# Kernel tuning notes

Hardware: AMD Instinct MI355X
Metric: run time of the kernel (lower is better)

Reference implementation:

```python
import jax, jax.numpy as jnp
import numpy as np

V, D, H, L, FF, BS = 50257, 1024, 16, 8, 4096, 1024
B, T = 2, 1024
HD = D // H
SCALE = 1.0 / np.sqrt(HD)
STD = 0.02


def setup_inputs() -> dict:
    key = jax.random.key(0)
    ks = jax.random.split(key, 8)
    rn = lambda k, s: (jax.random.normal(k, s, jnp.float32) * STD)
    return {
        'idx': jax.random.randint(ks[0], (B, T), 0, V),
        'tok_emb': rn(ks[1], (V, D)),
        'pos_emb': rn(ks[2], (1, BS, D)),
        'ln1_w': jnp.ones((L, D)), 'ln1_b': jnp.zeros((L, D)),
        'qkv_w': rn(ks[3], (L, 3 * D, D)), 'qkv_b': jnp.zeros((L, 3 * D)),
        'proj_w': rn(ks[4], (L, D, D)), 'proj_b': jnp.zeros((L, D)),
        'ln2_w': jnp.ones((L, D)), 'ln2_b': jnp.zeros((L, D)),
        'fc1_w': rn(ks[5], (L, FF, D)), 'fc1_b': jnp.zeros((L, FF)),
        'fc2_w': rn(ks[6], (L, D, FF)), 'fc2_b': jnp.zeros((L, D)),
        'lnf_w': jnp.ones((D,)), 'lnf_b': jnp.zeros((D,)),
    }


def layernorm(x, w, b, eps=1e-5):
    mu = jnp.mean(x, axis=-1, keepdims=True)
    var = jnp.mean(jnp.square(x - mu), axis=-1, keepdims=True)
    return (x - mu) * jax.lax.rsqrt(var + eps) * w + b


def _forward(idx, tok_emb, pos_emb, ln1_w, ln1_b, qkv_w, qkv_b, proj_w, proj_b,
             ln2_w, ln2_b, fc1_w, fc1_b, fc2_w, fc2_b, lnf_w, lnf_b):
    b, t = idx.shape
    x = tok_emb[idx] + pos_emb[0, :t]           # [B,T,D]; dropout identity in eval
    mask = jnp.tril(jnp.ones((t, t), dtype=bool))  # causal

    def block(x, p):
        l1w, l1b, qw, qb, pw, pb, l2w, l2b, f1w, f1b, f2w, f2b = p
        h = layernorm(x, l1w, l1b)
        qkv = h @ qw.T + qb                      # [B,T,3D]
        qkv = qkv.reshape(b, t, 3, H, HD)
        q, k, v = qkv[:, :, 0], qkv[:, :, 1], qkv[:, :, 2]  # [B,T,H,HD]
        att = jnp.einsum('bqhd,bkhd->bhqk', q, k) * SCALE
        att = jnp.where(mask, att, -jnp.inf)
        att = jax.nn.softmax(att, axis=-1)       # attn dropout identity in eval
        y = jnp.einsum('bhqk,bkhd->bqhd', att, v).reshape(b, t, D)
        x = x + (y @ pw.T + pb)
        h = layernorm(x, l2w, l2b)
        h = jax.nn.gelu(h @ f1w.T + f1b, approximate=False)  # exact GELU as nn.GELU
        x = x + (h @ f2w.T + f2b)
        return x, None

    params = (ln1_w, ln1_b, qkv_w, qkv_b, proj_w, proj_b,
              ln2_w, ln2_b, fc1_w, fc1_b, fc2_w, fc2_b)
    x, _ = jax.lax.scan(block, x, params)
    x = layernorm(x, lnf_w, lnf_b)
    logits = x @ tok_emb.T                       # weight-tied head
    return logits


def reference(idx, tok_emb, pos_emb, ln1_w, ln1_b, qkv_w, qkv_b, proj_w, proj_b,
              ln2_w, ln2_b, fc1_w, fc1_b, fc2_w, fc2_b, lnf_w, lnf_b):
    return _forward(idx, tok_emb, pos_emb, ln1_w, ln1_b, qkv_w, qkv_b, proj_w,
                    proj_b, ln2_w, ln2_b, fc1_w, fc1_b, fc2_w, fc2_b, lnf_w, lnf_b)
```

## Files before the change

### kernel.cpp

```cpp
#include <hip/hip_runtime.h>
#include <cstdint>

#define Dm 1024
#define Tm 1024
#define Bm 2
#define Lm 8
#define FFm 4096
#define Vm 50257
#define Mm (Bm * Tm)
#define VPAD2 50432

typedef __bf16 bf16x8 __attribute__((ext_vector_type(8)));
typedef float f32x4 __attribute__((ext_vector_type(4)));
typedef unsigned short u16;
typedef unsigned int u32;
typedef u16 u16x8 __attribute__((ext_vector_type(8)));
typedef u16 u16x4 __attribute__((ext_vector_type(4)));

__device__ __forceinline__ u16 f2bf(float f) {
  u32 u = __float_as_uint(f);
  u += 0x7FFFu + ((u >> 16) & 1u);
  return (u16)(u >> 16);
}
__device__ __forceinline__ float bf2f(u16 u) {
  return __uint_as_float((u32)u << 16);
}
__device__ __forceinline__ u32 packbf(float lo, float hi) {
  return (u32)f2bf(lo) | ((u32)f2bf(hi) << 16);
}

__device__ __forceinline__ void gload16(const u16* g, u16* l) {
  __builtin_amdgcn_global_load_lds(
      (const __attribute__((address_space(1))) void*)g,
      (__attribute__((address_space(3))) void*)l, 16, 0, 0);
}

__global__ __launch_bounds__(256) void embed_k(
    const int* __restrict__ idx, const float* __restrict__ tok,
    const float* __restrict__ pos, float* __restrict__ x) {
  int m = blockIdx.x, t = threadIdx.x;
  int id = idx[m];
  int tt = m & (Tm - 1);
  float4 a = *(const float4*)(tok + (size_t)id * Dm + t * 4);
  float4 p = *(const float4*)(pos + (size_t)tt * Dm + t * 4);
  float4 o;
  o.x = a.x + p.x; o.y = a.y + p.y; o.z = a.z + p.z; o.w = a.w + p.w;
  *(float4*)(x + (size_t)m * Dm + t * 4) = o;
}

__global__ __launch_bounds__(256) void conv_k(const float* __restrict__ s,
                                              u16* __restrict__ d,
                                              long long nsrc, long long ntot) {
  long long i = ((long long)blockIdx.x * 256 + threadIdx.x) * 8;
  if (i >= ntot) return;
  u16x8 r = {0, 0, 0, 0, 0, 0, 0, 0};
  if (i < nsrc) {
    float4 a = *(const float4*)(s + i);
    float4 b = *(const float4*)(s + i + 4);
    r[0] = f2bf(a.x); r[1] = f2bf(a.y); r[2] = f2bf(a.z); r[3] = f2bf(a.w);
    r[4] = f2bf(b.x); r[5] = f2bf(b.y); r[6] = f2bf(b.z); r[7] = f2bf(b.w);
  }
  *(u16x8*)(d + i) = r;
}

#define R0 (3 * Dm * Dm)
#define R1 (Dm * Dm)
#define R2 (FFm * Dm)
#define R3 (Dm * FFm)
__global__ __launch_bounds__(256) void convw_k(
    const float* __restrict__ s0, const float* __restrict__ s1,
    const float* __restrict__ s2, const float* __restrict__ s3,
    u16* __restrict__ d) {
  size_t i = ((size_t)blockIdx.x * 256 + threadIdx.x) * 8;
  const float* s;
  size_t o;
  if (i < R0) { s = s0; o = i; }
  else if (i < (size_t)R0 + R1) { s = s1; o = i - R0; }
  else if (i < (size_t)R0 + R1 + R2) { s = s2; o = i - R0 - R1; }
  else { s = s3; o = i - R0 - R1 - R2; }
  float4 a = *(const float4*)(s + o);
  float4 b = *(const float4*)(s + o + 4);
  u16x8 r;
  r[0] = f2bf(a.x); r[1] = f2bf(a.y); r[2] = f2bf(a.z); r[3] = f2bf(a.w);
  r[4] = f2bf(b.x); r[5] = f2bf(b.y); r[6] = f2bf(b.z); r[7] = f2bf(b.w);
  *(u16x8*)(d + i) = r;
}

__global__ __launch_bounds__(256) void ln_k(const float* __restrict__ x,
                                            const float* __restrict__ w,
                                            const float* __restrict__ b,
                                            u16* __restrict__ out) {
  __shared__ float red[4];
  int row = blockIdx.x, t = threadIdx.x;
  float4 v = *(const float4*)(x + (size_t)row * Dm + t * 4);
  float s = v.x + v.y + v.z + v.w;
#pragma unroll
  for (int mm = 1; mm < 64; mm <<= 1) s += __shfl_xor(s, mm);
  if ((t & 63) == 0) red[t >> 6] = s;
  __syncthreads();
  float mu = (red[0] + red[1] + red[2] + red[3]) * (1.0f / Dm);
  __syncthreads();
  float dx = v.x - mu, dy = v.y - mu, dz = v.z - mu, dw = v.w - mu;
  float sq = dx * dx + dy * dy + dz * dz + dw * dw;
#pragma unroll
  for (int mm = 1; mm < 64; mm <<= 1) sq += __shfl_xor(sq, mm);
  if ((t & 63) == 0) red[t >> 6] = sq;
  __syncthreads();
  float var = (red[0] + red[1] + red[2] + red[3]) * (1.0f / Dm);
  float rs = rsqrtf(var + 1e-5f);
  float4 wv = *(const float4*)(w + t * 4);
  float4 bv = *(const float4*)(b + t * 4);
  u16x4 o;
  o[0] = f2bf(dx * rs * wv.x + bv.x);
  o[1] = f2bf(dy * rs * wv.y + bv.y);
  o[2] = f2bf(dz * rs * wv.z + bv.z);
  o[3] = f2bf(dw * rs * wv.w + bv.w);
  *(u16x4*)(out + (size_t)row * Dm + t * 4) = o;
}

__global__ __launch_bounds__(512, 2) void gemm8_k(
    const u16* __restrict__ A, const u16* __restrict__ W,
    const float* __restrict__ bias, float* __restrict__ Cf,
    u16* __restrict__ Cb, int ldc, int nstore, int K, int gelu, int mblks,
    int nblks) {
  __shared__ __align__(16) u16 As[4][8192];
  __shared__ __align__(16) u16 Ws[4][8192];
  int nwg = mblks * nblks;
  int orig = blockIdx.x;
  int q8 = nwg >> 3, r8 = nwg & 7, xcd = orig & 7, loc = orig >> 3;
  int wg = (xcd < r8 ? xcd * (q8 + 1) : r8 * (q8 + 1) + (xcd - r8) * q8) + loc;
  int bx = wg % mblks, by = wg / mblks;
  int m0 = bx << 8, n0 = by << 8;
  int t = threadIdx.x, wave = t >> 6, lane = t & 63;
  int wr = wave >> 2, wc = wave & 3;
  int lr = lane & 15, cq = lane >> 4;
  int row0 = t >> 2;
  int kcG = (t & 3) ^ ((t >> 3) & 3);
  const u16* gA = A + (size_t)(m0 + row0) * K + kcG * 8;
  const u16* gW = W + (size_t)(n0 + row0) * K + kcG * 8;
  size_t rstep = (size_t)128 * K;

  f32x4 acc[8][4] = {};
  int nch = K >> 5;

  for (int s = 0; s < 3; ++s) {
    gload16(gA + s * 32, &As[s][wave * 512]);
    gload16(gA + rstep + s * 32, &As[s][4096 + wave * 512]);
    gload16(gW + s * 32, &Ws[s][wave * 512]);
    gload16(gW + rstep + s * 32, &Ws[s][4096 + wave * 512]);
  }
  asm volatile("s_waitcnt vmcnt(8)" ::: "memory");
  __builtin_amdgcn_s_barrier();

  for (int c = 0; c < nch; ++c) {
    const u16* sA = As[c & 3];
    const u16* sW = Ws[c & 3];
    bf16x8 afr[4], bfr[4];
#pragma unroll
    for (int mi = 0; mi < 4; ++mi) {
      int rowm = wr * 128 + mi * 16 + lr;
      afr[mi] =
          *(const bf16x8*)&sA[rowm * 32 + ((cq ^ ((rowm >> 1) & 3)) << 3)];
    }
#pragma unroll
    for (int ni = 0; ni < 4; ++ni) {
      int rown = wc * 64 + ni * 16 + lr;
      bfr[ni] =
          *(const bf16x8*)&sW[rown * 32 + ((cq ^ ((rown >> 1) & 3)) << 3)];
    }
    if (c + 3 < nch) {
      int s3 = (c + 3) & 3;
      gload16(gA + (size_t)(c + 3) * 32, &As[s3][wave * 512]);
      gload16(gA + rstep + (size_t)(c + 3) * 32, &As[s3][4096 + wave * 512]);
    }
    __builtin_amdgcn_s_barrier();
    asm volatile("s_waitcnt lgkmcnt(0)" ::: "memory");
    __builtin_amdgcn_sched_barrier(0);
    __builtin_amdgcn_s_setprio(1);
#pragma unroll
    for (int mi = 0; mi < 4; ++mi)
#pragma unroll
      for (int ni = 0; ni < 4; ++ni)
        acc[mi][ni] = __builtin_amdgcn_mfma_f32_16x16x32_bf16(
            afr[mi], bfr[ni], acc[mi][ni], 0, 0, 0);
    __builtin_amdgcn_s_setprio(0);
    __builtin_amdgcn_s_barrier();
#pragma unroll
    for (int mi = 0; mi < 4; ++mi) {
      int rowm = wr * 128 + (mi + 4) * 16 + lr;
      afr[mi] =
          *(const bf16x8*)&sA[rowm * 32 + ((cq ^ ((rowm >> 1) & 3)) << 3)];
    }
    if (c + 3 < nch) {
      int s3 = (c + 3) & 3;
      gload16(gW + (size_t)(c + 3) * 32, &Ws[s3][wave * 512]);
      gload16(gW + rstep + (size_t)(c + 3) * 32, &Ws[s3][4096 + wave * 512]);
    }
    __builtin_amdgcn_s_barrier();
    asm volatile("s_waitcnt lgkmcnt(0)" ::: "memory");
    __builtin_amdgcn_sched_barrier(0);
    __builtin_amdgcn_s_setprio(1);
#pragma unroll
    for (int mi = 0; mi < 4; ++mi)
#pragma unroll
      for (int ni = 0; ni < 4; ++ni)
        acc[mi + 4][ni] = __builtin_amdgcn_mfma_f32_16x16x32_bf16(
            afr[mi], bfr[ni], acc[mi + 4][ni], 0, 0, 0);
    __builtin_amdgcn_s_setprio(0);
    if (c + 1 < nch) {
      if (c + 3 < nch)
        asm volatile("s_waitcnt vmcnt(8)" ::: "memory");
      else if (c + 2 < nch)
        asm volatile("s_waitcnt vmcnt(4)" ::: "memory");
      else
        asm volatile("s_waitcnt vmcnt(0)" ::: "memory");
    }
    __builtin_amdgcn_s_barrier();
  }

  int gm0 = m0 + wr * 128 + (cq << 2);
  int gn0 = n0 + wc * 64 + lr;
#pragma unroll
  for (int mi = 0; mi < 8; ++mi) {
#pragma unroll
    for (int ni = 0; ni < 4; ++ni) {
      int gm = gm0 + mi * 16;
      int gn = gn0 + ni * 16;
      if (gn < nstore) {
        float bv = bias ? bias[gn] : 0.f;
#pragma unroll
        for (int j = 0; j < 4; ++j) {
          float o = acc[mi][ni][j] + bv;
          if (gelu) o = 0.5f * o * (1.0f + erff(o * 0.70710678118654752f));
          if (Cb) Cb[(size_t)(gm + j) * ldc + gn] = f2bf(o);
          else Cf[(size_t)(gm + j) * ldc + gn] = o;
        }
      }
    }
  }
}

__global__ __launch_bounds__(256) void gemm_k(
    const u16* __restrict__ A, const u16* __restrict__ W,
    const float* __restrict__ bias, const float* __restrict__ res,
    float* __restrict__ Cf, u16* __restrict__ Cb, int ldc, int nstore, int K,
    int gelu, int mblks, int nblks) {
  __shared__ __align__(16) u16 As[2][4096];
  __shared__ __align__(16) u16 Ws[2][4096];
  int id = blockIdx.x;
  int c = id & 7, m2 = id >> 3;
  int bx = m2 % mblks;
  int by = (m2 / mblks) * 8 + c;
  if (by >= nblks) return;
  int m0 = bx << 7, n0 = by << 7;
  int t = threadIdx.x;
  int wave = t >> 6, lane = t & 63;
  int wm = (wave & 1) << 6, wn = (wave >> 1) << 6;
  int lr = lane & 15, cq = lane >> 4;

  f32x4 acc[4][4] = {};

  int ch0 = wave * 64 + lane;
  int ch1 = 256 + ch0;
  int r0 = ch0 >> 2, c0 = (ch0 & 3) ^ ((r0 >> 1) & 3);
  int r1 = ch1 >> 2, c1 = (ch1 & 3) ^ ((r1 >> 1) & 3);
  const u16* gA0 = A + (size_t)(m0 + r0) * K + c0 * 8;
  const u16* gA1 = A + (size_t)(m0 + r1) * K + c1 * 8;
  const u16* gW0 = W + (size_t)(n0 + r0) * K + c0 * 8;
  const u16* gW1 = W + (size_t)(n0 + r1) * K + c1 * 8;

  int nst = K >> 5;
  gload16(gA0, &As[0][wave * 512]);
  gload16(gA1, &As[0][2048 + wave * 512]);
  gload16(gW0, &Ws[0][wave * 512]);
  gload16(gW1, &Ws[0][2048 + wave * 512]);
  __syncthreads();

  for (int i = 0; i < nst; ++i) {
    int cur = i & 1;
    if (i + 1 < nst) {
      int ko = (i + 1) << 5;
      gload16(gA0 + ko, &As[cur ^ 1][wave * 512]);
      gload16(gA1 + ko, &As[cur ^ 1][2048 + wave * 512]);
      gload16(gW0 + ko, &Ws[cur ^ 1][wave * 512]);
      gload16(gW1 + ko, &Ws[cur ^ 1][2048 + wave * 512]);
    }
    bf16x8 af[4], bf[4];
#pragma unroll
    for (int mi = 0; mi < 4; ++mi) {
      int rr = wm + mi * 16 + lr;
      af[mi] =
          *(const bf16x8*)&As[cur][rr * 32 + ((cq ^ ((rr >> 1) & 3)) << 3)];
    }
#pragma unroll
    for (int ni = 0; ni < 4; ++ni) {
      int rr = wn + ni * 16 + lr;
      bf[ni] =
          *(const bf16x8*)&Ws[cur][rr * 32 + ((cq ^ ((rr >> 1) & 3)) << 3)];
    }
#pragma unroll
    for (int mi = 0; mi < 4; ++mi)
#pragma unroll
      for (int ni = 0; ni < 4; ++ni)
        acc[mi][ni] = __builtin_amdgcn_mfma_f32_16x16x32_bf16(
            af[mi], bf[ni], acc[mi][ni], 0, 0, 0);
    __syncthreads();
  }

  int orow = cq << 2, ocol = lr;
#pragma unroll
  for (int mi = 0; mi < 4; ++mi) {
#pragma unroll
    for (int ni = 0; ni < 4; ++ni) {
      int gm = m0 + wm + mi * 16 + orow;
      int gn = n0 + wn + ni * 16 + ocol;
      if (gn < nstore) {
        float bv = bias ? bias[gn] : 0.f;
#pragma unroll
        for (int j = 0; j < 4; ++j) {
          float o = acc[mi][ni][j] + bv;
          if (gelu) o = 0.5f * o * (1.0f + erff(o * 0.70710678118654752f));
          if (res) o += res[(size_t)(gm + j) * ldc + gn];
          if (Cb) Cb[(size_t)(gm + j) * ldc + gn] = f2bf(o);
          else Cf[(size_t)(gm + j) * ldc + gn] = o;
        }
      }
    }
  }
}

__global__ __launch_bounds__(256) void gemmsk_k(
    const u16* __restrict__ A, const u16* __restrict__ W,
    const float* __restrict__ bias, float* __restrict__ C, int ldc, int K,
    int klen, int mblks, int nblks) {
  __shared__ __align__(16) u16 As[2][4096];
  __shared__ __align__(16) u16 Ws[2][4096];
  int id = blockIdx.x;
  int bx = id % mblks;
  int tmp = id / mblks;
  int by = tmp % nblks;
  int ks = tmp / nblks;
  int m0 = bx << 7, n0 = by << 7;
  int koff = ks * klen;
  int t = threadIdx.x;
  int wave = t >> 6, lane = t & 63;
  int wm = (wave & 1) << 6, wn = (wave >> 1) << 6;
  int lr = lane & 15, cq = lane >> 4;

  f32x4 acc[4][4] = {};

  int ch0 = wave * 64 + lane;
  int ch1 = 256 + ch0;
  int r0 = ch0 >> 2, c0 = (ch0 & 3) ^ ((r0 >> 1) & 3);
  int r1 = ch1 >> 2, c1 = (ch1 & 3) ^ ((r1 >> 1) & 3);
  const u16* gA0 = A + (size_t)(m0 + r0) * K + koff + c0 * 8;
  const u16* gA1 = A + (size_t)(m0 + r1) * K + koff + c1 * 8;
  const u16* gW0 = W + (size_t)(n0 + r0) * K + koff + c0 * 8;
  const u16* gW1 = W + (size_t)(n0 + r1) * K + koff + c1 * 8;

  int nst = klen >> 5;
  gload16(gA0, &As[0][wave * 512]);
  gload16(gA1, &As[0][2048 + wave * 512]);
  gload16(gW0, &Ws[0][wave * 512]);
  gload16(gW1, &Ws[0][2048 + wave * 512]);
  __syncthreads();

  for (int i = 0; i < nst; ++i) {
    int cur = i & 1;
    if (i + 1 < nst) {
      int ko = (i + 1) << 5;
      gload16(gA0 + ko, &As[cur ^ 1][wave * 512]);
      gload16(gA1 + ko, &As[cur ^ 1][2048 + wave * 512]);
      gload16(gW0 + ko, &Ws[cur ^ 1][wave * 512]);
      gload16(gW1 + ko, &Ws[cur ^ 1][2048 + wave * 512]);
    }
    bf16x8 af[4], bf[4];
#pragma unroll
    for (int mi = 0; mi < 4; ++mi) {
      int rr = wm + mi * 16 + lr;
      af[mi] =
          *(const bf16x8*)&As[cur][rr * 32 + ((cq ^ ((rr >> 1) & 3)) << 3)];
    }
#pragma unroll
    for (int ni = 0; ni < 4; ++ni) {
      int rr = wn + ni * 16 + lr;
      bf[ni] =
          *(const bf16x8*)&Ws[cur][rr * 32 + ((cq ^ ((rr >> 1) & 3)) << 3)];
    }
#pragma unroll
    for (int mi = 0; mi < 4; ++mi)
#pragma unroll
      for (int ni = 0; ni < 4; ++ni)
        acc[mi][ni] = __builtin_amdgcn_mfma_f32_16x16x32_bf16(
            af[mi], bf[ni], acc[mi][ni], 0, 0, 0);
    __syncthreads();
  }

  int orow = cq << 2, ocol = lr;
#pragma unroll
  for (int mi = 0; mi < 4; ++mi) {
#pragma unroll
    for (int ni = 0; ni < 4; ++ni) {
      int gm = m0 + wm + mi * 16 + orow;
      int gn = n0 + wn + ni * 16 + ocol;
      float bv = (ks == 0) ? bias[gn] : 0.f;
#pragma unroll
      for (int j = 0; j < 4; ++j)
        atomicAdd(&C[(size_t)(gm + j) * ldc + gn], acc[mi][ni][j] + bv);
    }
  }
}

__global__ __launch_bounds__(256) void vtr_k(const u16* __restrict__ qkv,
                                             u16* __restrict__ vt) {
  __shared__ u16 T[64 * 68];
  int bh = blockIdx.y;
  int b = bh >> 4, h = bh & 15;
  int t0 = blockIdx.x << 6;
  int tid = threadIdx.x;
  int r = tid >> 2, q4 = tid & 3;
  const u16* src = qkv + (size_t)(b * Tm + t0 + r) * 3072 + 2048 + h * 64 +
                   q4 * 16;
  *(u16x8*)&T[r * 68 + q4 * 16] = *(const u16x8*)src;
  *(u16x8*)&T[r * 68 + q4 * 16 + 8] = *(const u16x8*)(src + 8);
  __syncthreads();
  int dr = tid >> 2, kq = tid & 3;
  u16x8 o0, o1;
#pragma unroll
  for (int u = 0; u < 8; ++u) o0[u] = T[(kq * 16 + u) * 68 + dr];
#pragma unroll
  for (int u = 0; u < 8; ++u) o1[u] = T[(kq * 16 + 8 + u) * 68 + dr];
  u16* dst = vt + ((size_t)bh * 64 + dr) * 1024 + t0 + kq * 16;
  *(u16x8*)dst = o0;
  *(u16x8*)(dst + 8) = o1;
}

__global__ __launch_bounds__(256) void attn_k(const u16* __restrict__ qkv,
                                              const u16* __restrict__ vt,
                                              u16* __restrict__ y) {
  __shared__ __align__(16) u16 Ks[2][4096];
  __shared__ __align__(16) u16 Vs[2][4096];
  int qt = gridDim.x - 1 - blockIdx.x;
  int q0 = qt << 6;
  int bh = blockIdx.y;
  int b = bh >> 4, h = bh & 15;
  int t = threadIdx.x, wave = t >> 6, lane = t & 63;
  int lr = lane & 15, cq = lane >> 4;

  bf16x8 qf[2];
  {
    size_t base = (size_t)(b * Tm + q0 + wave * 16 + lr) * 3072 + h * 64;
#pragma unroll
    for (int ks = 0; ks < 2; ++ks) {
      u16x8 qa = *(const u16x8*)(qkv + base + ks * 32 + cq * 8);
#pragma unroll
      for (int u = 0; u < 8; ++u) qa[u] = f2bf(bf2f(qa[u]) * 0.125f);
      qf[ks] = *(bf16x8*)&qa;
    }
  }

  f32x4 accO[4] = {};
  float m_run = -1e30f, l_run = 0.f;

  int ch0 = wave * 64 + lane, ch1 = 256 + ch0;
  int kr0 = ch0 >> 3, kc0 = ((ch0 & 7) ^ (kr0 & 7)) << 3;
  int kr1 = ch1 >> 3, kc1 = ((ch1 & 7) ^ (kr1 & 7)) << 3;
  const u16* kbase = qkv + (size_t)b * Tm * 3072 + 1024 + h * 64;
  const u16* vbase = vt + (size_t)bh * 64 * 1024;

  {
    gload16(kbase + (size_t)kr0 * 3072 + kc0, &Ks[0][wave * 512]);
    gload16(kbase + (size_t)kr1 * 3072 + kc1, &Ks[0][2048 + wave * 512]);
    gload16(vbase + (size_t)kr0 * 1024 + kc0, &Vs[0][wave * 512]);
    gload16(vbase + (size_t)kr1 * 1024 + kc1, &Vs[0][2048 + wave * 512]);
  }
  __syncthreads();

  for (int tk = 0; tk <= qt; ++tk) {
    int cur = tk & 1;
    if (tk < qt) {
      int kb0 = (tk + 1) << 6;
      gload16(kbase + (size_t)(kb0 + kr0) * 3072 + kc0,
              &Ks[cur ^ 1][wave * 512]);
      gload16(kbase + (size_t)(kb0 + kr1) * 3072 + kc1,
              &Ks[cur ^ 1][2048 + wave * 512]);
      gload16(vbase + (size_t)kr0 * 1024 + kb0 + kc0,
              &Vs[cur ^ 1][wave * 512]);
      gload16(vbase + (size_t)kr1 * 1024 + kb0 + kc1,
              &Vs[cur ^ 1][2048 + wave * 512]);
    }

    f32x4 s[4] = {};
    __builtin_amdgcn_s_setprio(1);
#pragma unroll
    for (int ks = 0; ks < 2; ++ks)
#pragma unroll
      for (int ni = 0; ni < 4; ++ni) {
        int rk = ni * 16 + lr;
        int ck = ks * 4 + cq;
        bf16x8 kf = *(const bf16x8*)&Ks[cur][rk * 64 + ((ck ^ (rk & 7)) << 3)];
        s[ni] = __builtin_amdgcn_mfma_f32_16x16x32_bf16(kf, qf[ks], s[ni],
                                                        0, 0, 0);
      }
    __builtin_amdgcn_s_setprio(0);

    if (tk == qt) {
      int kb0 = tk << 6;
      int qa = q0 + wave * 16 + lr;
#pragma unroll
      for (int ni = 0; ni < 4; ++ni)
#pragma unroll
        for (int r = 0; r < 4; ++r)
          if (kb0 + ni * 16 + cq * 4 + r > qa) s[ni][r] = -1e30f;
    }

    float mx = fmaxf(fmaxf(s[0][0], s[0][1]), fmaxf(s[0][2], s[0][3]));
#pragma unroll
    for (int ni = 1; ni < 4; ++ni)
      mx = fmaxf(mx, fmaxf(fmaxf(s[ni][0], s[ni][1]),
                           fmaxf(s[ni][2], s[ni][3])));
    mx = fmaxf(mx, __shfl_xor(mx, 16));
    mx = fmaxf(mx, __shfl_xor(mx, 32));
    float mn = fmaxf(m_run, mx);
    float alpha = __expf(m_run - mn);
    m_run = mn;
    float ls = 0.f;
    u32 packed[4][2];
#pragma unroll
    for (int ni = 0; ni < 4; ++ni) {
      float p0 = __expf(s[ni][0] - mn), p1 = __expf(s[ni][1] - mn);
      float p2 = __expf(s[ni][2] - mn), p3 = __expf(s[ni][3] - mn);
      ls += (p0 + p1) + (p2 + p3);
      packed[ni][0] = packbf(p0, p1);
      packed[ni][1] = packbf(p2, p3);
    }
    ls += __shfl_xor(ls, 16);
    ls += __shfl_xor(ls, 32);
    l_run = l_run * alpha + ls;

#pragma unroll
    for (int j = 0; j < 4; ++j) {
      float a = __shfl(alpha, (cq << 2) + j);
#pragma unroll
      for (int di = 0; di < 4; ++di) accO[di][j] *= a;
    }

    bf16x8 pf[2];
#pragma unroll
    for (int ks2 = 0; ks2 < 2; ++ks2) {
      union { u32 w[4]; bf16x8 v; } pu;
#pragma unroll
      for (int w = 0; w < 4; ++w) {
        int src = lr + 16 * (((cq & 1) << 1) + (w >> 1));
        int a = __shfl((int)packed[2 * ks2][w & 1], src);
        int bb = __shfl((int)packed[2 * ks2 + 1][w & 1], src);
        pu.w[w] = (cq >> 1) ? (u32)bb : (u32)a;
      }
      pf[ks2] = pu.v;
    }

    __builtin_amdgcn_s_setprio(1);
#pragma unroll
    for (int ks2 = 0; ks2 < 2; ++ks2)
#pragma unroll
      for (int di = 0; di < 4; ++di) {
        int rv = di * 16 + lr;
        int ck = ks2 * 4 + cq;
        bf16x8 vf = *(const bf16x8*)&Vs[cur][rv * 64 + ((ck ^ (rv & 7)) << 3)];
        accO[di] = __builtin_amdgcn_mfma_f32_16x16x32_bf16(pf[ks2], vf,
                                                           accO[di], 0, 0, 0);
      }
    __builtin_amdgcn_s_setprio(0);
    __syncthreads();
  }

  float iv = 1.0f / l_run;
  int qrow = q0 + wave * 16 + (cq << 2);
#pragma unroll
  for (int j = 0; j < 4; ++j) {
    float ivj = __shfl(iv, (cq << 2) + j);
    size_t row = (size_t)(b * Tm + qrow + j) * Dm + h * 64;
#pragma unroll
    for (int di = 0; di < 4; ++di)
      y[row + di * 16 + lr] = f2bf(accO[di][j] * ivj);
  }
}

#define WELEMS ((size_t)(R0 + R1 + R2 + R3))

static inline void launch_gemm(const u16* A, const u16* W, const float* bias,
                               const float* res, float* Cf, u16* Cb, int ldc,
                               int nstore, int K, int gelu, int mblks,
                               int nblks, hipStream_t stream) {
  int gx = 8 * mblks * ((nblks + 7) / 8);
  gemm_k<<<gx, 256, 0, stream>>>(A, W, bias, res, Cf, Cb, ldc, nstore, K,
                                 gelu, mblks, nblks);
}

extern "C" void kernel_launch(void* const* d_in, const int* in_sizes, int n_in,
                              void* d_out, int out_size, void* d_ws,
                              size_t ws_size, hipStream_t stream) {
  const int* idx = (const int*)d_in[0];
  const float* tok = (const float*)d_in[1];
  const float* pos = (const float*)d_in[2];
  const float* ln1w = (const float*)d_in[3];
  const float* ln1b = (const float*)d_in[4];
  const float* qkvw = (const float*)d_in[5];
  const float* qkvb = (const float*)d_in[6];
  const float* projw = (const float*)d_in[7];
  const float* projb = (const float*)d_in[8];
  const float* ln2w = (const float*)d_in[9];
  const float* ln2b = (const float*)d_in[10];
  const float* fc1w = (const float*)d_in[11];
  const float* fc1b = (const float*)d_in[12];
  const float* fc2w = (const float*)d_in[13];
  const float* fc2b = (const float*)d_in[14];
  const float* lnfw = (const float*)d_in[15];
  const float* lnfb = (const float*)d_in[16];
  float* out = (float*)d_out;

  char* w = (char*)d_ws;
  float* x = (float*)w;  w += (size_t)Mm * Dm * 4;
  u16* h = (u16*)w;      w += (size_t)Mm * Dm * 2;
  u16* big = (u16*)w;    w += (size_t)Mm * FFm * 2;
  u16* vtG = (u16*)w;    w += (size_t)Bm * 16 * 64 * Tm * 2;
  u16* wbuf = (u16*)w;   w += WELEMS * 2;
  u16* tokbf = (u16*)w;
  size_t need_full = (size_t)(w - (char*)d_ws) + (size_t)VPAD2 * Dm * 2;
  bool full = ws_size >= need_full;

  embed_k<<<Mm, 256, 0, stream>>>(idx, tok, pos, x);

  if (full) {
    long long nsrc = (long long)Vm * Dm, ntot = (long long)VPAD2 * Dm;
    conv_k<<<(int)((ntot + 2047) / 2048), 256, 0, stream>>>(tok, tokbf, nsrc,
                                                            ntot);
  }

  for (int l = 0; l < Lm; ++l) {
    convw_k<<<(int)(WELEMS / 2048), 256, 0, stream>>>(
        qkvw + (size_t)l * R0, projw + (size_t)l * R1, fc1w + (size_t)l * R2,
        fc2w + (size_t)l * R3, wbuf);
    ln_k<<<Mm, 256, 0, stream>>>(x, ln1w + l * Dm, ln1b + l * Dm, h);
    launch_gemm(h, wbuf, qkvb + (size_t)l * 3 * Dm, nullptr, nullptr, big,
                3 * Dm, 3 * Dm, Dm, 0, Mm / 128, (3 * Dm) / 128, stream);
    vtr_k<<<dim3(Tm / 64, Bm * 16), 256, 0, stream>>>(big, vtG);
    attn_k<<<dim3(Tm / 64, Bm * 16), 256, 0, stream>>>(big, vtG, h);
    gemmsk_k<<<Mm / 128 * (Dm / 128) * 2, 256, 0, stream>>>(
        h, wbuf + R0, projb + (size_t)l * Dm, x, Dm, Dm, Dm / 2, Mm / 128,
        Dm / 128);
    ln_k<<<Mm, 256, 0, stream>>>(x, ln2w + l * Dm, ln2b + l * Dm, h);
    gemm8_k<<<(Mm / 256) * (FFm / 256), 512, 0, stream>>>(
        h, wbuf + R0 + R1, fc1b + (size_t)l * FFm, nullptr, big, FFm, FFm,
        Dm, 1, Mm / 256, FFm / 256);
    gemmsk_k<<<Mm / 128 * (Dm / 128) * 4, 256, 0, stream>>>(
        big, wbuf + R0 + R1 + R2, fc2b + (size_t)l * Dm, x, Dm, FFm, FFm / 4,
        Mm / 128, Dm / 128);
  }

  ln_k<<<Mm, 256, 0, stream>>>(x, lnfw, lnfb, h);

  if (full) {
    gemm8_k<<<(Mm / 256) * (VPAD2 / 256), 512, 0, stream>>>(
        h, tokbf, nullptr, out, nullptr, Vm, Vm, Dm, 0, Mm / 256,
        VPAD2 / 256);
  } else {
    for (int c0 = 0; c0 < VPAD2; c0 += 6400) {
      int rows = VPAD2 - c0 < 6400 ? VPAD2 - c0 : 6400;
      long long nsrc = (long long)(Vm - c0 < rows ? (Vm - c0 > 0 ? Vm - c0 : 0)
                                                  : rows) *
                       Dm;
      long long ntot = (long long)rows * Dm;
      conv_k<<<(int)((ntot + 2047) / 2048), 256, 0, stream>>>(
          tok + (size_t)c0 * Dm, wbuf, nsrc, ntot);
      launch_gemm(h, wbuf, nullptr, nullptr, out + c0, nullptr, Vm, Vm - c0,
                  Dm, 0, Mm / 128, rows / 128, stream);
    }
  }
}
```

Before: 2.168 ms.

## Add 128x256 tile GEMM for QKV and FC1, restructure gemm8 LDS reads

Adds a gemm8h_k variant with a 128x256 output tile (half the M rows per workgroup) and uses it for the QKV and FC1 projections, replacing the generic launch_gemm and the 256x256 gemm8_k. The smaller tile doubles the number of workgroups for these M=2048 GEMMs so more CUs are busy, at the cost of less operand reuse per tile. gemm8_k is also reworked: all A fragments for both halves are loaded up front with a precomputed swizzle offset, one barrier is removed, and it waits on a partial lgkmcnt so the first MFMA half can start earlier. The inline asm waits drop their memory clobbers and sched_barriers, which relies on the compiler not reordering LDS reads across them.

```diff
diff --git a/kernel.cpp b/kernel.cpp
--- a/kernel.cpp
+++ b/kernel.cpp
@@ -134,6 +134,7 @@
   int t = threadIdx.x, wave = t >> 6, lane = t & 63;
   int wr = wave >> 2, wc = wave & 3;
   int lr = lane & 15, cq = lane >> 4;
+  int sw8 = (cq ^ ((lr >> 1) & 3)) << 3;
   int row0 = t >> 2;
   int kcG = (t & 3) ^ ((t >> 3) & 3);
   const u16* gA = A + (size_t)(m0 + row0) * K + kcG * 8;
@@ -149,71 +150,60 @@
     gload16(gW + s * 32, &Ws[s][wave * 512]);
     gload16(gW + rstep + s * 32, &Ws[s][4096 + wave * 512]);
   }
-  asm volatile("s_waitcnt vmcnt(8)" ::: "memory");
+  asm volatile("s_waitcnt vmcnt(8)");
   __builtin_amdgcn_s_barrier();
 
   for (int c = 0; c < nch; ++c) {
     const u16* sA = As[c & 3];
     const u16* sW = Ws[c & 3];
-    bf16x8 afr[4], bfr[4];
-#pragma unroll
-    for (int mi = 0; mi < 4; ++mi) {
-      int rowm = wr * 128 + mi * 16 + lr;
-      afr[mi] =
-          *(const bf16x8*)&sA[rowm * 32 + ((cq ^ ((rowm >> 1) & 3)) << 3)];
-    }
-#pragma unroll
-    for (int ni = 0; ni < 4; ++ni) {
-      int rown = wc * 64 + ni * 16 + lr;
-      bfr[ni] =
-          *(const bf16x8*)&sW[rown * 32 + ((cq ^ ((rown >> 1) & 3)) << 3)];
-    }
+    bf16x8 afA[4], bfr[4], afB[4];
+#pragma unroll
+    for (int mi = 0; mi < 4; ++mi)
+      afA[mi] = *(const bf16x8*)&sA[(wr * 128 + mi * 16 + lr) * 32 + sw8];
+#pragma unroll
+    for (int ni = 0; ni < 4; ++ni)
+      bfr[ni] = *(const bf16x8*)&sW[(wc * 64 + ni * 16 + lr) * 32 + sw8];
+#pragma unroll
+    for (int mi = 0; mi < 4; ++mi)
+      afB[mi] =
+          *(const bf16x8*)&sA[(wr * 128 + (mi + 4) * 16 + lr) * 32 + sw8];
     if (c + 3 < nch) {
       int s3 = (c + 3) & 3;
       gload16(gA + (size_t)(c + 3) * 32, &As[s3][wave * 512]);
       gload16(gA + rstep + (size_t)(c + 3) * 32, &As[s3][4096 + wave * 512]);
     }
     __builtin_amdgcn_s_barrier();
-    asm volatile("s_waitcnt lgkmcnt(0)" ::: "memory");
-    __builtin_amdgcn_sched_barrier(0);
+    asm volatile("s_waitcnt lgkmcnt(4)");
     __builtin_amdgcn_s_setprio(1);
 #pragma unroll
     for (int mi = 0; mi < 4; ++mi)
 #pragma unroll
       for (int ni = 0; ni < 4; ++ni)
         acc[mi][ni] = __builtin_amdgcn_mfma_f32_16x16x32_bf16(
-            afr[mi], bfr[ni], acc[mi][ni], 0, 0, 0);
+            afA[mi], bfr[ni], acc[mi][ni], 0, 0, 0);
     __builtin_amdgcn_s_setprio(0);
     __builtin_amdgcn_s_barrier();
-#pragma unroll
-    for (int mi = 0; mi < 4; ++mi) {
-      int rowm = wr * 128 + (mi + 4) * 16 + lr;
-      afr[mi] =
-          *(const bf16x8*)&sA[rowm * 32 + ((cq ^ ((rowm >> 1) & 3)) << 3)];
-    }
     if (c + 3 < nch) {
       int s3 = (c + 3) & 3;
       gload16(gW + (size_t)(c + 3) * 32, &Ws[s3][wave * 512]);
       gload16(gW + rstep + (size_t)(c + 3) * 32, &Ws[s3][4096 + wave * 512]);
     }
-    __builtin_amdgcn_s_barrier();
-    asm volatile("s_waitcnt lgkmcnt(0)" ::: "memory");
-    __builtin_amdgcn_sched_barrier(0);
+    asm volatile("s_waitcnt lgkmcnt(0)");
     __builtin_amdgcn_s_setprio(1);
 #pragma unroll
     for (int mi = 0; mi < 4; ++mi)
 #pragma unroll
       for (int ni = 0; ni < 4; ++ni)
         acc[mi + 4][ni] = __builtin_amdgcn_mfma_f32_16x16x32_bf16(
-            afr[mi], bfr[ni], acc[mi + 4][ni], 0, 0, 0);
+            afB[mi], bfr[ni], acc[mi + 4][ni], 0, 0, 0);
     __builtin_amdgcn_s_setprio(0);
     if (c + 1 < nch) {
       if (c + 3 < nch)
-        asm volatile("s_waitcnt vmcnt(8)" ::: "memory");
+        asm volatile("s_waitcnt vmcnt(8)");
       else if (c + 2 < nch)
-        asm volatile("s_waitcnt vmcnt(4)" ::: "memory");
+        asm volatile("s_waitcnt vmcnt(4)");
       else
-        asm volatile("s_waitcnt vmcnt(0)" ::: "memory");
+        asm volatile("s_waitcnt vmcnt(0)");
     }
     __builtin_amdgcn_s_barrier();
   }
@@ -222,6 +212,99 @@
   int gn0 = n0 + wc * 64 + lr;
 #pragma unroll
   for (int mi = 0; mi < 8; ++mi) {
+#pragma unroll
+    for (int ni = 0; ni < 4; ++ni) {
+      int gm = gm0 + mi * 16;
+      int gn = gn0 + ni * 16;
+      if (gn < nstore) {
+        float bv = bias ? bias[gn] : 0.f;
+#pragma unroll
+        for (int j = 0; j < 4; ++j) {
+          float o = acc[mi][ni][j] + bv;
+          if (gelu) o = 0.5f * o * (1.0f + erff(o * 0.70710678118654752f));
+          if (Cb) Cb[(size_t)(gm + j) * ldc + gn] = f2bf(o);
+          else Cf[(size_t)(gm + j) * ldc + gn] = o;
+        }
+      }
+    }
+  }
+}
+
+__global__ __launch_bounds__(512, 2) void gemm8h_k(
+    const u16* __restrict__ A, const u16* __restrict__ W,
+    const float* __restrict__ bias, float* __restrict__ Cf,
+    u16* __restrict__ Cb, int ldc, int nstore, int K, int gelu, int mblks,
+    int nblks) {
+  __shared__ __align__(16) u16 As[4][4096];
+  __shared__ __align__(16) u16 Ws[4][8192];
+  int nwg = mblks * nblks;
+  int orig = blockIdx.x;
+  int q8 = nwg >> 3, r8 = nwg & 7, xcd = orig & 7, loc = orig >> 3;
+  int wg = (xcd < r8 ? xcd * (q8 + 1) : r8 * (q8 + 1) + (xcd - r8) * q8) + loc;
+  int bx = wg % mblks, by = wg / mblks;
+  int m0 = bx << 7, n0 = by << 8;
+  int t = threadIdx.x, wave = t >> 6, lane = t & 63;
+  int wr = wave >> 2, wc = wave & 3;
+  int lr = lane & 15, cq = lane >> 4;
+  int sw8 = (cq ^ ((lr >> 1) & 3)) << 3;
+  int row0 = t >> 2;
+  int kcG = (t & 3) ^ ((t >> 3) & 3);
+  const u16* gA = A + (size_t)(m0 + row0) * K + kcG * 8;
+  const u16* gW = W + (size_t)(n0 + row0) * K + kcG * 8;
+  size_t rstep = (size_t)128 * K;
+
+  f32x4 acc[4][4] = {};
+  int nch = K >> 5;
+
+  for (int s = 0; s < 3; ++s) {
+    gload16(gA + s * 32, &As[s][wave * 512]);
+    gload16(gW + s * 32, &Ws[s][wave * 512]);
+    gload16(gW + rstep + s * 32, &Ws[s][4096 + wave * 512]);
+  }
+  asm volatile("s_waitcnt vmcnt(6)");
+  __builtin_amdgcn_s_barrier();
+
+  for (int c = 0; c < nch; ++c) {
+    const u16* sA = As[c & 3];
+    const u16* sW = Ws[c & 3];
+    bf16x8 af[4], bf[4];
+#pragma unroll
+    for (int mi = 0; mi < 4; ++mi)
+      af[mi] = *(const bf16x8*)&sA[(wr * 64 + mi * 16 + lr) * 32 + sw8];
+#pragma unroll
+    for (int ni = 0; ni < 4; ++ni)
+      bf[ni] = *(const bf16x8*)&sW[(wc * 64 + ni * 16 + lr) * 32 + sw8];
+    if (c + 3 < nch) {
+      int s3 = (c + 3) & 3;
+      gload16(gA + (size_t)(c + 3) * 32, &As[s3][wave * 512]);
+      gload16(gW + (size_t)(c + 3) * 32, &Ws[s3][wave * 512]);
+      gload16(gW + rstep + (size_t)(c + 3) * 32, &Ws[s3][4096 + wave * 512]);
+    }
+    __builtin_amdgcn_s_barrier();
+    asm volatile("s_waitcnt lgkmcnt(0)");
+    __builtin_amdgcn_s_setprio(1);
+#pragma unroll
+    for (int mi = 0; mi < 4; ++mi)
+#pragma unroll
+      for (int ni = 0; ni < 4; ++ni)
+        acc[mi][ni] = __builtin_amdgcn_mfma_f32_16x16x32_bf16(
+            af[mi], bf[ni], acc[mi][ni], 0, 0, 0);
+    __builtin_amdgcn_s_setprio(0);
+    if (c + 1 < nch) {
+      if (c + 3 < nch)
+        asm volatile("s_waitcnt vmcnt(6)");
+      else if (c + 2 < nch)
+        asm volatile("s_waitcnt vmcnt(3)");
+      else
+        asm volatile("s_waitcnt vmcnt(0)");
+    }
+    __builtin_amdgcn_s_barrier();
+  }
+
+  int gm0 = m0 + wr * 64 + (cq << 2);
+  int gn0 = n0 + wc * 64 + lr;
+#pragma unroll
+  for (int mi = 0; mi < 4; ++mi) {
 #pragma unroll
     for (int ni = 0; ni < 4; ++ni) {
       int gm = gm0 + mi * 16;
@@ -642,17 +725,18 @@
         qkvw + (size_t)l * R0, projw + (size_t)l * R1, fc1w + (size_t)l * R2,
         fc2w + (size_t)l * R3, wbuf);
     ln_k<<<Mm, 256, 0, stream>>>(x, ln1w + l * Dm, ln1b + l * Dm, h);
-    launch_gemm(h, wbuf, qkvb + (size_t)l * 3 * Dm, nullptr, nullptr, big,
-                3 * Dm, 3 * Dm, Dm, 0, Mm / 128, (3 * Dm) / 128, stream);
+    gemm8h_k<<<(Mm / 128) * ((3 * Dm) / 256), 512, 0, stream>>>(
+        h, wbuf, qkvb + (size_t)l * 3 * Dm, nullptr, big, 3 * Dm, 3 * Dm, Dm,
+        0, Mm / 128, (3 * Dm) / 256);
     vtr_k<<<dim3(Tm / 64, Bm * 16), 256, 0, stream>>>(big, vtG);
     attn_k<<<dim3(Tm / 64, Bm * 16), 256, 0, stream>>>(big, vtG, h);
     gemmsk_k<<<Mm / 128 * (Dm / 128) * 2, 256, 0, stream>>>(
         h, wbuf + R0, projb + (size_t)l * Dm, x, Dm, Dm, Dm / 2, Mm / 128,
         Dm / 128);
     ln_k<<<Mm, 256, 0, stream>>>(x, ln2w + l * Dm, ln2b + l * Dm, h);
-    gemm8_k<<<(Mm / 256) * (FFm / 256), 512, 0, stream>>>(
+    gemm8h_k<<<(Mm / 128) * (FFm / 256), 512, 0, stream>>>(
         h, wbuf + R0 + R1, fc1b + (size_t)l * FFm, nullptr, big, FFm, FFm,
-        Dm, 1, Mm / 256, FFm / 256);
+        Dm, 1, Mm / 128, FFm / 256);
     gemmsk_k<<<Mm / 128 * (Dm / 128) * 4, 256, 0, stream>>>(
         big, wbuf + R0 + R1 + R2, fc2b + (size_t)l * Dm, x, Dm, FFm, FFm / 4,
         Mm / 128, Dm / 128);
```

Measured after the change: 1.982 ms. 1.09x faster.

## Shrink 512-thread GEMM tile to 128x256 and use it for QKV

Applied to the files above, without the earlier changes.

The 256x256 GEMM kernel becomes a 128x256 tile kernel. Each K-chunk now needs a single A-fragment load and one MFMA phase instead of two half-phases with extra barriers, and LDS use for A is halved. The QKV projection moves from the generic launch_gemm to this kernel. FC1 and the LM head also use it. The smaller tile gives more workgroups and better occupancy and CU balance, but each tile reuses less data, so more global and L2 traffic is needed per FLOP.

```diff
diff --git a/kernel.cpp b/kernel.cpp
--- a/kernel.cpp
+++ b/kernel.cpp
@@ -34,6 +34,8 @@
       (const __attribute__((address_space(1))) void*)g,
       (__attribute__((address_space(3))) void*)l, 16, 0, 0);
 }
+
+#define WTV(N) asm volatile("s_waitcnt vmcnt(" #N ")")
 
 __global__ __launch_bounds__(256) void embed_k(
     const int* __restrict__ idx, const float* __restrict__ tok,
@@ -118,110 +120,81 @@
   *(u16x4*)(out + (size_t)row * Dm + t * 4) = o;
 }
 
-__global__ __launch_bounds__(512, 2) void gemm8_k(
+__global__ __launch_bounds__(512, 2) void gemm8h_k(
     const u16* __restrict__ A, const u16* __restrict__ W,
     const float* __restrict__ bias, float* __restrict__ Cf,
     u16* __restrict__ Cb, int ldc, int nstore, int K, int gelu, int mblks,
     int nblks) {
-  __shared__ __align__(16) u16 As[4][8192];
+  __shared__ __align__(16) u16 As[4][4096];
   __shared__ __align__(16) u16 Ws[4][8192];
   int nwg = mblks * nblks;
   int orig = blockIdx.x;
   int q8 = nwg >> 3, r8 = nwg & 7, xcd = orig & 7, loc = orig >> 3;
   int wg = (xcd < r8 ? xcd * (q8 + 1) : r8 * (q8 + 1) + (xcd - r8) * q8) + loc;
   int bx = wg % mblks, by = wg / mblks;
-  int m0 = bx << 8, n0 = by << 8;
+  int m0 = bx << 7, n0 = by << 8;
   int t = threadIdx.x, wave = t >> 6, lane = t & 63;
   int wr = wave >> 2, wc = wave & 3;
   int lr = lane & 15, cq = lane >> 4;
+  int sw8 = (cq ^ ((lr >> 1) & 3)) << 3;
   int row0 = t >> 2;
   int kcG = (t & 3) ^ ((t >> 3) & 3);
   const u16* gA = A + (size_t)(m0 + row0) * K + kcG * 8;
   const u16* gW = W + (size_t)(n0 + row0) * K + kcG * 8;
   size_t rstep = (size_t)128 * K;
 
-  f32x4 acc[8][4] = {};
+  f32x4 acc[4][4] = {};
   int nch = K >> 5;
 
   for (int s = 0; s < 3; ++s) {
     gload16(gA + s * 32, &As[s][wave * 512]);
-    gload16(gA + rstep + s * 32, &As[s][4096 + wave * 512]);
     gload16(gW + s * 32, &Ws[s][wave * 512]);
     gload16(gW + rstep + s * 32, &Ws[s][4096 + wave * 512]);
   }
-  asm volatile("s_waitcnt vmcnt(8)" ::: "memory");
+  WTV(6);
   __builtin_amdgcn_s_barrier();
 
   for (int c = 0; c < nch; ++c) {
     const u16* sA = As[c & 3];
     const u16* sW = Ws[c & 3];
-    bf16x8 afr[4], bfr[4];
-#pragma unroll
-    for (int mi = 0; mi < 4; ++mi) {
-      int rowm = wr * 128 + mi * 16 + lr;
-      afr[mi] =
-          *(const bf16x8*)&sA[rowm * 32 + ((cq ^ ((rowm >> 1) & 3)) << 3)];
-    }
-#pragma unroll
-    for (int ni = 0; ni < 4; ++ni) {
-      int rown = wc * 64 + ni * 16 + lr;
-      bfr[ni] =
-          *(const bf16x8*)&sW[rown * 32 + ((cq ^ ((rown >> 1) & 3)) << 3)];
-    }
+    bf16x8 af[4], bf[4];
+#pragma unroll
+    for (int mi = 0; mi < 4; ++mi)
+      af[mi] = *(const bf16x8*)&sA[(wr * 64 + mi * 16 + lr) * 32 + sw8];
+#pragma unroll
+    for (int ni = 0; ni < 4; ++ni)
+      bf[ni] = *(const bf16x8*)&sW[(wc * 64 + ni * 16 + lr) * 32 + sw8];
     if (c + 3 < nch) {
       int s3 = (c + 3) & 3;
       gload16(gA + (size_t)(c + 3) * 32, &As[s3][wave * 512]);
-      gload16(gA + rstep + (size_t)(c + 3) * 32, &As[s3][4096 + wave * 512]);
+      gload16(gW + (size_t)(c + 3) * 32, &Ws[s3][wave * 512]);
+      gload16(gW + rstep + (size_t)(c + 3) * 32, &Ws[s3][4096 + wave * 512]);
     }
     __builtin_amdgcn_s_barrier();
-    asm volatile("s_waitcnt lgkmcnt(0)" ::: "memory");
-    __builtin_amdgcn_sched_barrier(0);
+    asm volatile("s_waitcnt lgkmcnt(0)");
     __builtin_amdgcn_s_setprio(1);
 #pragma unroll
     for (int mi = 0; mi < 4; ++mi)
 #pragma unroll
       for (int ni = 0; ni < 4; ++ni)
         acc[mi][ni] = __builtin_amdgcn_mfma_f32_16x16x32_bf16(
-            afr[mi], bfr[ni], acc[mi][ni], 0, 0, 0);
-    __builtin_amdgcn_s_setprio(0);
-    __builtin_amdgcn_s_barrier();
-#pragma unroll
-    for (int mi = 0; mi < 4; ++mi) {
-      int rowm = wr * 128 + (mi + 4) * 16 + lr;
-      afr[mi] =
-          *(const bf16x8*)&sA[rowm * 32 + ((cq ^ ((rowm >> 1) & 3)) << 3)];
-    }
-    if (c + 3 < nch) {
-      int s3 = (c + 3) & 3;
-      gload16(gW + (size_t)(c + 3) * 32, &Ws[s3][wave * 512]);
-      gload16(gW + rstep + (size_t)(c + 3) * 32, &Ws[s3][4096 + wave * 512]);
-    }
-    __builtin_amdgcn_s_barrier();
-    asm volatile("s_waitcnt lgkmcnt(0)" ::: "memory");
-    __builtin_amdgcn_sched_barrier(0);
-    __builtin_amdgcn_s_setprio(1);
-#pragma unroll
-    for (int mi = 0; mi < 4; ++mi)
-#pragma unroll
-      for (int ni = 0; ni < 4; ++ni)
-        acc[mi + 4][ni] = __builtin_amdgcn_mfma_f32_16x16x32_bf16(
-            afr[mi], bfr[ni], acc[mi + 4][ni], 0, 0, 0);
+            af[mi], bf[ni], acc[mi][ni], 0, 0, 0);
     __builtin_amdgcn_s_setprio(0);
     if (c + 1 < nch) {
       if (c + 3 < nch)
-        asm volatile("s_waitcnt vmcnt(8)" ::: "memory");
+        WTV(6);
       else if (c + 2 < nch)
-        asm volatile("s_waitcnt vmcnt(4)" ::: "memory");
+        WTV(3);
       else
-        asm volatile("s_waitcnt vmcnt(0)" ::: "memory");
+        WTV(0);
     }
     __builtin_amdgcn_s_barrier();
   }
 
-  int gm0 = m0 + wr * 128 + (cq << 2);
+  int gm0 = m0 + wr * 64 + (cq << 2);
   int gn0 = n0 + wc * 64 + lr;
 #pragma unroll
-  for (int mi = 0; mi < 8; ++mi) {
+  for (int mi = 0; mi < 4; ++mi) {
 #pragma unroll
     for (int ni = 0; ni < 4; ++ni) {
       int gm = gm0 + mi * 16;
@@ -642,17 +615,18 @@
         qkvw + (size_t)l * R0, projw + (size_t)l * R1, fc1w + (size_t)l * R2,
         fc2w + (size_t)l * R3, wbuf);
     ln_k<<<Mm, 256, 0, stream>>>(x, ln1w + l * Dm, ln1b + l * Dm, h);
-    launch_gemm(h, wbuf, qkvb + (size_t)l * 3 * Dm, nullptr, nullptr, big,
-                3 * Dm, 3 * Dm, Dm, 0, Mm / 128, (3 * Dm) / 128, stream);
+    gemm8h_k<<<(Mm / 128) * ((3 * Dm) / 256), 512, 0, stream>>>(
+        h, wbuf, qkvb + (size_t)l * 3 * Dm, nullptr, big, 3 * Dm, 3 * Dm, Dm,
+        0, Mm / 128, (3 * Dm) / 256);
     vtr_k<<<dim3(Tm / 64, Bm * 16), 256, 0, stream>>>(big, vtG);
     attn_k<<<dim3(Tm / 64, Bm * 16), 256, 0, stream>>>(big, vtG, h);
     gemmsk_k<<<Mm / 128 * (Dm / 128) * 2, 256, 0, stream>>>(
         h, wbuf + R0, projb + (size_t)l * Dm, x, Dm, Dm, Dm / 2, Mm / 128,
         Dm / 128);
     ln_k<<<Mm, 256, 0, stream>>>(x, ln2w + l * Dm, ln2b + l * Dm, h);
-    gemm8_k<<<(Mm / 256) * (FFm / 256), 512, 0, stream>>>(
+    gemm8h_k<<<(Mm / 128) * (FFm / 256), 512, 0, stream>>>(
         h, wbuf + R0 + R1, fc1b + (size_t)l * FFm, nullptr, big, FFm, FFm,
-        Dm, 1, Mm / 256, FFm / 256);
+        Dm, 1, Mm / 128, FFm / 256);
     gemmsk_k<<<Mm / 128 * (Dm / 128) * 4, 256, 0, stream>>>(
         big, wbuf + R0 + R1 + R2, fc2b + (size_t)l * Dm, x, Dm, FFm, FFm / 4,
         Mm / 128, Dm / 128);
@@ -661,8 +635,8 @@
   ln_k<<<Mm, 256, 0, stream>>>(x, lnfw, lnfb, h);
 
   if (full) {
-    gemm8_k<<<(Mm / 256) * (VPAD2 / 256), 512, 0, stream>>>(
-        h, tokbf, nullptr, out, nullptr, Vm, Vm, Dm, 0, Mm / 256,
+    gemm8h_k<<<(Mm / 128) * (VPAD2 / 256), 512, 0, stream>>>(
+        h, tokbf, nullptr, out, nullptr, Vm, Vm, Dm, 0, Mm / 128,
         VPAD2 / 256);
   } else {
     for (int c0 = 0; c0 < VPAD2; c0 += 6400) {
```

After: 2.032 ms. 1.07x faster.
